# Kernel optimization log

Hardware: AMD Instinct MI355X
Metric: run time of the kernel (lower is better)

## Reference

```python
import jax, jax.numpy as jnp
import numpy as np

B = 1024
D = 128  # in_out_dim


def _lin(k, i, o):
    return jax.random.normal(k, (i, o), jnp.float32) / np.sqrt(i)


def setup_inputs() -> dict:
    key = jax.random.key(0)
    ks = jax.random.split(key, 24)
    inp = {
        'pseudo_t': jax.random.uniform(ks[0], (), jnp.float32),
        'x': jax.random.normal(ks[1], (B, D), jnp.float32),
        'g_x': jax.random.normal(ks[2], (B, 1), jnp.float32),
        'p': jax.random.uniform(ks[3], (B, 1), jnp.float32),
        # GRN encoder: 128->1024->960->896 (Tanh), decoder 896->128
        'gw0': _lin(ks[4], 128, 1024), 'gb0': jnp.zeros((1024,), jnp.float32),
        'gw1': _lin(ks[5], 1024, 960), 'gb1': jnp.zeros((960,), jnp.float32),
        'gw2': _lin(ks[6], 960, 896), 'gb2': jnp.zeros((896,), jnp.float32),
        'gdw': _lin(ks[7], 896, 128), 'gdb': jnp.zeros((128,), jnp.float32),
        # BRD encoder: 129->512->448 (Tanh), decoder 448->1
        'bw0': _lin(ks[8], 129, 512), 'bb0': jnp.zeros((512,), jnp.float32),
        'bw1': _lin(ks[9], 512, 448), 'bb1': jnp.zeros((448,), jnp.float32),
        'bdw': _lin(ks[10], 448, 1), 'bdb': jnp.zeros((1,), jnp.float32),
    }
    return inp


def reference(pseudo_t, x, g_x, p, gw0, gb0, gw1, gb1, gw2, gb2, gdw, gdb,
              bw0, bb0, bw1, bb1, bdw, bdb):
    bsz = x.shape[0]
    x_gene = x[:, :-1]                       # [B, D-1]
    s = jnp.full((bsz, 1), pseudo_t, x.dtype)

    def grn(state):                          # [..., D] -> [..., D]
        h = jnp.tanh(state @ gw0 + gb0)
        h = jnp.tanh(h @ gw1 + gb1)
        h = jnp.tanh(h @ gw2 + gb2)
        return h @ gdw + gdb

    dx_dt = grn(jnp.concatenate([s, x_gene], axis=1))   # [B, D]

    # BRD growth function g(x, t)
    st = jnp.concatenate([s, x], axis=1)                # [B, D+1]
    e = jnp.tanh(st @ bw0 + bb0)
    e = jnp.tanh(e @ bw1 + bb1)
    g = e @ bdw + bdb                                   # [B, 1]

    # trace of d(dx_dt[:, :D-1]) / d(x_gene), per sample (CNF divergence)
    s_scalar = jnp.reshape(pseudo_t, (1,)).astype(x.dtype)

    def f_single(xg_i):                                 # [D-1] -> [D]
        return grn(jnp.concatenate([s_scalar, xg_i]))

    jac = jax.vmap(jax.jacfwd(f_single))(x_gene)        # [B, D, D-1]
    tr = jnp.trace(jac[:, :D - 1, :], axis1=1, axis2=2) # [B]

    dp_dt = g - p * tr[:, None]                         # [B, 1]
    return (dx_dt, g, dp_dt)
```

## Files before the change

kernel.cpp:

```cpp
#include <hip/hip_runtime.h>


typedef __bf16 bf16;
typedef __bf16 bf16x8 __attribute__((ext_vector_type(8)));
typedef float floatx4 __attribute__((ext_vector_type(4)));

#if defined(__has_builtin)
#if __has_builtin(__builtin_amdgcn_global_load_lds)
#define HAVE_GLL 1
#endif
#endif

typedef __attribute__((address_space(3))) char lds_char_t;
typedef __attribute__((address_space(1))) const char gbl_char_t;

__device__ inline void async_load16(const void* gp, void* lp) {
#ifdef HAVE_GLL
  __builtin_amdgcn_global_load_lds((gbl_char_t*)gp, (lds_char_t*)lp, 16, 0, 0);
#else
  *(bf16x8*)lp = *(const bf16x8*)gp;
#endif
}

__device__ inline void stage_async(const bf16* src, long row0, int ld, int kc,
                                   bf16* dst, int wid, int sr8, int cph) {
#pragma unroll
  for (int t = 0; t < 4; ++t) {
    const int r = (wid * 4 + t) * 8 + sr8;
    const int csrc = (cph - r) & 7;
    async_load16(src + (row0 + r) * (size_t)ld + kc + csrc * 8,
                 dst + r * 64 + cph * 8);
  }
}

__device__ inline void mfma_block(const bf16* As, const bf16* Bs,
                                  floatx4 (&acc)[4][4], int wm, int wn,
                                  int l16, int quad) {
#pragma unroll
  for (int ks = 0; ks < 2; ++ks) {
    bf16x8 af[4], bfv[4];
#pragma unroll
    for (int mt = 0; mt < 4; ++mt) {
      const int r = wm * 64 + mt * 16 + l16;
      const int c = (ks * 4 + quad + r) & 7;
      af[mt] = *(const bf16x8*)(As + r * 64 + c * 8);
    }
#pragma unroll
    for (int nt = 0; nt < 4; ++nt) {
      const int r = wn * 64 + nt * 16 + l16;
      const int c = (ks * 4 + quad + r) & 7;
      bfv[nt] = *(const bf16x8*)(Bs + r * 64 + c * 8);
    }
#pragma unroll
    for (int mt = 0; mt < 4; ++mt)
#pragma unroll
      for (int nt = 0; nt < 4; ++nt)
        acc[mt][nt] = __builtin_amdgcn_mfma_f32_16x16x32_bf16(af[mt], bfv[nt], acc[mt][nt], 0, 0, 0);
  }
}

struct TB1 {
  const bf16* A;
  const bf16* w0b;
  const bf16* d0b;
  const bf16* sc;
  bf16* Upr;
  int i0, NT, ch, nTiles;
};

struct TB2 {
  const bf16* A;
  const bf16* Bm;
  const bf16* sc;
  const float* gdw;
  float* tr;
  int i0, NT, ch, nTiles;
};

__device__ __forceinline__ void gemm256(const bf16* Aop, const bf16* Bop,
                                        int m0, int n0, int NT, char* lds,
                                        floatx4 (&acc)[8][4]) {
  const int tid = threadIdx.x;
  const int wid = tid >> 6, lane = tid & 63;
  const int wm = wid & 1, wn = wid >> 1;
  const int quad = lane >> 4, l16 = lane & 15;

  const int sr = tid >> 2;
  const int sg = tid & 3;
  const int csrc = (sg - (sr >> 1)) & 3;
  const bf16* aSrc = Aop + (size_t)(m0 + sr) * 1024 + csrc * 8;
  const bf16* bSrc = Bop + (size_t)(n0 + sr) * 1024 + csrc * 8;

  const int rA = wm * 128 + l16;
  const int rB = wn * 64 + l16;
  const int aOff = rA * 64 + ((quad + (rA >> 1)) & 3) * 16;
  const int bOff = rB * 64 + ((quad + (rB >> 1)) & 3) * 16;

#define STAGE4(hh)                                                             \
  {                                                                            \
    char* db = lds + ((hh) & 3) * 32768;                                       \
    const int kce = (hh) * 32;                                                 \
    async_load16(aSrc + kce, db + tid * 16);                                   \
    async_load16(aSrc + 131072 + kce, db + 8192 + tid * 16);                   \
    async_load16(bSrc + kce, db + 16384 + tid * 16);                           \
    async_load16(bSrc + 131072 + kce, db + 24576 + tid * 16);                  \
  }

#define HALF_COMPUTE(HB)                                                       \
  {                                                                            \
    const char* hb_ = (const char*)(HB);                                       \
    bf16x8 af[8], bv[4];                                                       \
    _Pragma("unroll")                                                          \
    for (int nf = 0; nf < 4; ++nf)                                             \
      bv[nf] = *(const bf16x8*)(hb_ + 16384 + bOff + nf * 1024);               \
    _Pragma("unroll")                                                          \
    for (int mf = 0; mf < 8; ++mf)                                             \
      af[mf] = *(const bf16x8*)(hb_ + aOff + mf * 1024);                       \
    _Pragma("unroll")                                                          \
    for (int mf = 0; mf < 8; ++mf)                                             \
      _Pragma("unroll")                                                        \
      for (int nf = 0; nf < 4; ++nf)                                           \
        acc[mf][nf] = __builtin_amdgcn_mfma_f32_16x16x32_bf16(                 \
            af[mf], bv[nf], acc[mf][nf], 0, 0, 0);                             \
  }

#define VMW(N) asm volatile("s_waitcnt vmcnt(" #N ")" ::: "memory")
#define BARRIER()                                                              \
  asm volatile("s_barrier" ::: "memory");                                      \
  __builtin_amdgcn_sched_barrier(0)

  STAGE4(0);
  STAGE4(1);
  VMW(4);
  BARRIER();

#pragma unroll 2
  for (int t = 0; t < NT; ++t) {
    const int h0 = 2 * t;
    const bool more = (t + 1 < NT);

    if (more) STAGE4(h0 + 2);
    HALF_COMPUTE(lds + (h0 & 3) * 32768);
    if (more) VMW(4); else VMW(0);
    BARRIER();

    if (more) STAGE4(h0 + 3);
    HALF_COMPUTE(lds + ((h0 + 1) & 3) * 32768);
    if (more) {
      VMW(4);
      BARRIER();
    }
  }
#undef STAGE4
#undef HALF_COMPUTE
#undef VMW
#undef BARRIER
}

__device__ __forceinline__ void gemm256_b1(const bf16* Aop, const bf16* w0p,
                                           const bf16* d0p1, const bf16* d0p2,
                                           int m0, int NT, char* lds,
                                           floatx4 (&acc)[8][4]) {
  const int tid = threadIdx.x;
  const int wid = tid >> 6, lane = tid & 63;
  const int wm = wid & 1, wn = wid >> 1;
  const int quad = lane >> 4, l16 = lane & 15;

  const int sr = tid >> 2;
  const int sg = tid & 3;
  const int csrc = (sg - (sr >> 1)) & 3;
  const bf16* aSrc = Aop + (size_t)(m0 + sr) * 1024 + csrc * 8;

  const int rA = wm * 128 + l16;
  const int rB = wn * 64 + l16;
  const int aOff = rA * 64 + ((quad + (rA >> 1)) & 3) * 16;
  const int bOff = rB * 64 + ((quad + (rB >> 1)) & 3) * 16;

#define STAGE1(hh)                                                             \
  {                                                                            \
    char* db = lds + ((hh) & 3) * 32768;                                       \
    const int kce = (hh) * 32;                                                 \
    bf16x8 wv = *(const bf16x8*)(w0p + kce);                                   \
    bf16x8 v1 = *(const bf16x8*)(d0p1 + kce);                                  \
    bf16x8 v2 = *(const bf16x8*)(d0p2 + kce);                                  \
    async_load16(aSrc + kce, db + tid * 16);                                   \
    async_load16(aSrc + 131072 + kce, db + 8192 + tid * 16);                   \
    bf16x8 o1, o2;                                                             \
    _Pragma("unroll")                                                          \
    for (int k = 0; k < 8; ++k) {                                              \
      o1[k] = (bf16)((float)wv[k] * (float)v1[k]);                             \
      o2[k] = (bf16)((float)wv[k] * (float)v2[k]);                             \
    }                                                                          \
    *(bf16x8*)(db + 16384 + tid * 16) = o1;                                    \
    *(bf16x8*)(db + 24576 + tid * 16) = o2;                                    \
  }

#define HALF_COMPUTE(HB)                                                       \
  {                                                                            \
    const char* hb_ = (const char*)(HB);                                       \
    bf16x8 af[8], bv[4];                                                       \
    _Pragma("unroll")                                                          \
    for (int nf = 0; nf < 4; ++nf)                                             \
      bv[nf] = *(const bf16x8*)(hb_ + 16384 + bOff + nf * 1024);               \
    _Pragma("unroll")                                                          \
    for (int mf = 0; mf < 8; ++mf)                                             \
      af[mf] = *(const bf16x8*)(hb_ + aOff + mf * 1024);                       \
    _Pragma("unroll")                                                          \
    for (int mf = 0; mf < 8; ++mf)                                             \
      _Pragma("unroll")                                                        \
      for (int nf = 0; nf < 4; ++nf)                                           \
        acc[mf][nf] = __builtin_amdgcn_mfma_f32_16x16x32_bf16(                 \
            af[mf], bv[nf], acc[mf][nf], 0, 0, 0);                             \
  }

#define VMW(N) asm volatile("s_waitcnt vmcnt(" #N ")" ::: "memory")
#define BARRIER1()                                                             \
  asm volatile("s_waitcnt lgkmcnt(0)\ns_barrier" ::: "memory");                \
  __builtin_amdgcn_sched_barrier(0)

  STAGE1(0);
  STAGE1(1);
  VMW(2);
  BARRIER1();

#pragma unroll 2
  for (int t = 0; t < NT; ++t) {
    const int h0 = 2 * t;
    const bool more = (t + 1 < NT);

    if (more) STAGE1(h0 + 2);
    HALF_COMPUTE(lds + (h0 & 3) * 32768);
    if (more) VMW(2); else VMW(0);
    BARRIER1();

    if (more) STAGE1(h0 + 3);
    HALF_COMPUTE(lds + ((h0 + 1) & 3) * 32768);
    if (more) {
      VMW(2);
      BARRIER1();
    }
  }
#undef STAGE1
#undef HALF_COMPUTE
#undef VMW
#undef BARRIER1
}

__global__ __launch_bounds__(512, 2) void kt8_b1(TB1 p) {
  extern __shared__ __align__(16) char lds[];
  const int bid = blockIdx.x;
  const int nt  = ((bid >> 4) << 3) | (bid & 7);
  const int mtp = (bid >> 3) & 1;
  if (nt >= p.nTiles) return;

  const int tid = threadIdx.x;
  const int wid = tid >> 6, lane = tid & 63;
  const int wm = wid & 1, wn = wid >> 1;
  const int quad = lane >> 4, l16 = lane & 15;
  const long nLim = (long)p.ch * 128;

  const int sr = tid >> 2;
  const int sg = tid & 3;
  const int csrc = (sg - (sr >> 1)) & 3;
  const int wsel = (sr == 127) ? 127 : sr + 1;
  const bf16* w0p  = p.w0b + wsel * 1024 + csrc * 8;
  const bf16* d0p1 = p.d0b + (size_t)(p.i0 + nt * 2) * 1024 + csrc * 8;
  const bf16* d0p2 = d0p1 + 1024;

#pragma unroll 1
  for (int q = 0; q < 2; ++q) {
    const int mt = mtp * 2 + q;
    floatx4 acc[8][4];
#pragma unroll
    for (int a = 0; a < 8; ++a)
#pragma unroll
      for (int b = 0; b < 4; ++b)
#pragma unroll
        for (int r = 0; r < 4; ++r) acc[a][b][r] = 0.0f;

    gemm256_b1(p.A, w0p, d0p1, d0p2, mt * 256, p.NT, lds, acc);

    const int mb = mt * 256 + wm * 128;
#pragma unroll
    for (int nf = 0; nf < 4; ++nf) {
      const long n = (long)nt * 256 + wn * 64 + nf * 16 + l16;
      if (n < nLim) {
        const int ig = p.i0 + (int)(n >> 7);
        const bf16* dp = p.sc + (size_t)ig * 960;
        bf16* urow = p.Upr + (size_t)n * 1024;
#pragma unroll
        for (int mf = 0; mf < 8; ++mf) {
          const int mg = mb + mf * 16 + quad * 4;
          if (mg < 960) {
            union { bf16 h[4]; uint2 u; } o;
#pragma unroll
            for (int r = 0; r < 4; ++r)
              o.h[r] = (bf16)(acc[mf][nf][r] * (float)dp[mg + r]);
            *(uint2*)(urow + mg) = o.u;
          }
        }
      }
    }
  }
}

__global__ __launch_bounds__(512, 2) void kt8_b2(TB2 p) {
  extern __shared__ __align__(16) char lds[];
  const int bid = blockIdx.x;
  const int mt  = (bid >> 3) & 3;
  const int ntp = ((bid >> 5) << 3) | (bid & 7);
  const int npairs = (p.nTiles + 1) >> 1;
  if (ntp >= npairs) return;

  const int tid = threadIdx.x;
  const int wid = tid >> 6, lane = tid & 63;
  const int wm = wid & 1, wn = wid >> 1;
  const int quad = lane >> 4, l16 = lane & 15;
  const long nLim = (long)p.ch * 128;
  const int mb = mt * 256 + wm * 128;

  float sAB[2] = {0.0f, 0.0f};
#pragma unroll 1
  for (int q = 0; q < 2; ++q) {
    const int nt = ntp * 2 + q;
    if (nt >= p.nTiles) break;
    floatx4 acc[8][4];
#pragma unroll
    for (int a = 0; a < 8; ++a)
#pragma unroll
      for (int b = 0; b < 4; ++b)
#pragma unroll
        for (int r = 0; r < 4; ++r) acc[a][b][r] = 0.0f;

    gemm256(p.A, p.Bm, mt * 256, nt * 256, p.NT, lds, acc);

    float s = 0.0f;
#pragma unroll
    for (int nf = 0; nf < 4; ++nf) {
      const long n = (long)nt * 256 + wn * 64 + nf * 16 + l16;
      const int d = (int)(n & 127);
      if (n < nLim && d < 127) {
        const int ig = p.i0 + (int)(n >> 7);
        const bf16* dp = p.sc + (size_t)ig * 896;
#pragma unroll
        for (int mf = 0; mf < 8; ++mf) {
          const int mg = mb + mf * 16 + quad * 4;
          if (mg < 896) {
#pragma unroll
            for (int r = 0; r < 4; ++r) {
              const float w = (float)dp[mg + r] * p.gdw[(mg + r) * 128 + d];
              s += acc[mf][nf][r] * w;
            }
          }
        }
      }
    }
#pragma unroll
    for (int off = 1; off < 64; off <<= 1) s += __shfl_xor(s, off, 64);
    sAB[q] = s;
  }

  float* red = (float*)lds;
  if (lane == 0) { red[wid] = sAB[0]; red[8 + wid] = sAB[1]; }
  __syncthreads();
  const int ig0 = p.i0 + ntp * 4;
  if (tid == 0) {
    atomicAdd(p.tr + ig0, red[0] + red[1] + red[2] + red[3]);
    if (ntp * 2 + 1 < p.nTiles)
      atomicAdd(p.tr + ig0 + 2, red[8] + red[9] + red[10] + red[11]);
  }
  if (tid == 256) {
    atomicAdd(p.tr + ig0 + 1, red[4] + red[5] + red[6] + red[7]);
    if (ntp * 2 + 1 < p.nTiles)
      atomicAdd(p.tr + ig0 + 3, red[12] + red[13] + red[14] + red[15]);
  }
}

struct FArgs {
  const bf16* A; int lda;
  const bf16* Bt; int ldb;
  const float* bias;
  bf16* C; int ldc;
  bf16* D; int ldd;
  float* outF; int ldo;
  int K; int realN; int gridX;
};

template <int ACT>
__device__ inline void fwd_body(const FArgs& p, int bx, bf16* As, bf16* Bs) {
  const int tid  = threadIdx.x;
  const int wid  = tid >> 6, lane = tid & 63;
  const int wm   = wid & 1, wn = wid >> 1;
  const int quad = lane >> 4, l16 = lane & 15;
  const int sr8  = lane >> 3, cph = lane & 7;
  const int m0   = (bx % p.gridX) * 128;
  const int bn0  = (bx / p.gridX) * 128;

  floatx4 acc[4][4];
#pragma unroll
  for (int a = 0; a < 4; ++a)
#pragma unroll
    for (int b = 0; b < 4; ++b)
#pragma unroll
      for (int r = 0; r < 4; ++r) acc[a][b][r] = 0.0f;

  for (int kc = 0; kc < p.K; kc += 64) {
    stage_async(p.A, m0, p.lda, kc, As, wid, sr8, cph);
    stage_async(p.Bt, bn0, p.ldb, kc, Bs, wid, sr8, cph);
    __syncthreads();
    mfma_block(As, Bs, acc, wm, wn, l16, quad);
    __syncthreads();
  }

#pragma unroll
  for (int nt = 0; nt < 4; ++nt) {
    const int ng = bn0 + wn * 64 + nt * 16 + l16;
    const float bv = (ng < p.realN) ? p.bias[ng] : 0.0f;
#pragma unroll
    for (int mt = 0; mt < 4; ++mt)
#pragma unroll
      for (int r = 0; r < 4; ++r) {
        const int i = m0 + wm * 64 + mt * 16 + quad * 4 + r;
        const float v = acc[mt][nt][r] + bv;
        if (ACT) {
          const float t = tanhf(v);
          p.C[(size_t)i * p.ldc + ng] = (ng < p.realN) ? (bf16)t : (bf16)0.0f;
          if (p.D && ng < p.realN)
            p.D[(size_t)i * p.ldd + ng] = (bf16)(1.0f - t * t);
        } else if (ng < p.realN) {
          p.outF[(size_t)i * p.ldo + ng] = v;
        }
      }
  }
}

__global__ __launch_bounds__(256) void kt_fwd2(FArgs a, int na, FArgs b) {
  __shared__ __align__(16) bf16 As[8192];
  __shared__ __align__(16) bf16 Bs[8192];
  const int bx = blockIdx.x;
  if (bx < na) fwd_body<1>(a, bx, As, Bs);
  else         fwd_body<1>(b, bx - na, As, Bs);
}

__global__ __launch_bounds__(256) void kt_fwd1(FArgs a) {
  __shared__ __align__(16) bf16 As[8192];
  __shared__ __align__(16) bf16 Bs[8192];
  fwd_body<1>(a, blockIdx.x, As, Bs);
}

__global__ __launch_bounds__(256) void kt_dxgdot(FArgs a, int na,
                                                 const bf16* e1b, const float* bdw,
                                                 const float* bdb, float* gf,
                                                 float* gout) {
  __shared__ __align__(16) bf16 As[8192];
  __shared__ __align__(16) bf16 Bs[8192];
  const int bx = blockIdx.x;
  if (bx < na) { fwd_body<0>(a, bx, As, Bs); return; }
  const int i = (bx - na) * 4 + (threadIdx.x >> 6);
  const int lane = threadIdx.x & 63;
  float s = 0.0f;
  for (int k = lane; k < 448; k += 64) s += (float)e1b[(size_t)i * 512 + k] * bdw[k];
#pragma unroll
  for (int off = 32; off > 0; off >>= 1) s += __shfl_down(s, off, 64);
  if (lane == 0) {
    const float v = s + bdb[0];
    gf[i] = v;
    gout[i] = v;
  }
}

struct PArgs {
  const float *gw0, *gw1, *gw2, *gdw, *bw0, *bw1, *pt, *x;
  bf16 *gw0b, *gw0t, *gw1t, *gw2t, *gdwt, *bw0t, *bw1t, *Xg, *Xb;
};

__device__ inline void tpose_tile(bf16* dst, const float* src, int R, int C,
                                  int ldd, int tile, int tilesX, float* tl,
                                  int tid) {
  const int r0 = (tile % tilesX) * 64;
  const int c0 = (tile / tilesX) * 64;
  const int tx = tid & 63, ty0 = tid >> 6;
#pragma unroll
  for (int i = 0; i < 16; ++i) {
    const int ty = ty0 + i * 4;
    const int r = r0 + ty, c = c0 + tx;
    tl[ty * 65 + tx] = (r < R && c < C) ? src[(size_t)r * C + c] : 0.0f;
  }
  __syncthreads();
#pragma unroll
  for (int i = 0; i < 16; ++i) {
    const int ty = ty0 + i * 4;
    dst[(size_t)(c0 + ty) * ldd + r0 + tx] = (bf16)tl[tx * 65 + ty];
  }
}

__global__ __launch_bounds__(256) void kt_prep(PArgs p) {
  __shared__ float tl[64 * 65];
  int b = blockIdx.x;
  const int t = threadIdx.x;
  if (b < 512) { p.gw0b[b * 256 + t] = (bf16)p.gw0[b * 256 + t]; return; }
  b -= 512;
  if (b < 768) {
    const int idx = b * 256 + t;
    const int i = idx / 192, c = idx % 192;
    const float s = p.pt[0];
    float vb;
    if (c == 0) vb = s;
    else if (c <= 128) vb = p.x[i * 128 + c - 1];
    else vb = 0.0f;
    p.Xb[i * 192 + c] = (bf16)vb;
    if (c < 128) p.Xg[i * 128 + c] = (bf16)((c == 0) ? s : p.x[i * 128 + c - 1]);
    return;
  }
  b -= 768;
  if (b < 32)  { tpose_tile(p.gw0t, p.gw0, 128, 1024, 128, b, 2, tl, t);  return; }
  b -= 32;
  if (b < 256) { tpose_tile(p.gw1t, p.gw1, 1024, 960, 1024, b, 16, tl, t); return; }
  b -= 256;
  if (b < 256) { tpose_tile(p.gw2t, p.gw2, 960, 896, 1024, b, 16, tl, t); return; }
  b -= 256;
  if (b < 32)  { tpose_tile(p.gdwt, p.gdw, 896, 128, 1024, b, 16, tl, t); return; }
  b -= 32;
  if (b < 24)  { tpose_tile(p.bw0t, p.bw0, 129, 512, 192, b, 3, tl, t);  return; }
  b -= 24;
  if (b < 64)  { tpose_tile(p.bw1t, p.bw1, 512, 448, 512, b, 8, tl, t);  return; }
}

__global__ __launch_bounds__(256) void kt_fin(const float* gf, const float* tr,
                                              const float* pp, float* dp) {
  const int i = blockIdx.x * 256 + threadIdx.x;
  if (i < 1024) dp[i] = gf[i] - pp[i] * tr[i];
}

extern "C" void kernel_launch(void* const* d_in, const int* in_sizes, int n_in,
                              void* d_out, int out_size, void* d_ws, size_t ws_size,
                              hipStream_t stream) {
  const float* pt  = (const float*)d_in[0];
  const float* x   = (const float*)d_in[1];
  const float* pp  = (const float*)d_in[3];
  const float* gw0 = (const float*)d_in[4];
  const float* gb0 = (const float*)d_in[5];
  const float* gw1 = (const float*)d_in[6];
  const float* gb1 = (const float*)d_in[7];
  const float* gw2 = (const float*)d_in[8];
  const float* gb2 = (const float*)d_in[9];
  const float* gdw = (const float*)d_in[10];
  const float* gdb = (const float*)d_in[11];
  const float* bw0 = (const float*)d_in[12];
  const float* bb0 = (const float*)d_in[13];
  const float* bw1 = (const float*)d_in[14];
  const float* bb1 = (const float*)d_in[15];
  const float* bdw = (const float*)d_in[16];
  const float* bdb = (const float*)d_in[17];
  float* out = (float*)d_out;

  static bool s_attr = false;
  if (!s_attr) {
    hipFuncSetAttribute((const void*)kt8_b1,
                        hipFuncAttributeMaxDynamicSharedMemorySize, 131072);
    hipFuncSetAttribute((const void*)kt8_b2,
                        hipFuncAttributeMaxDynamicSharedMemorySize, 131072);
    s_attr = true;
  }

  char* w = (char*)d_ws;
  size_t used = 0;
  auto alloc = [&](size_t nbytes) -> void* {
    void* r = w + used;
    used += (nbytes + 255) & ~(size_t)255;
    return r;
  };
  bf16* gw0b = (bf16*)alloc((size_t)128 * 1024 * 2);
  bf16* gw0t = (bf16*)alloc((size_t)1024 * 128 * 2);
  bf16* gw1t = (bf16*)alloc((size_t)1024 * 1024 * 2);
  bf16* gw2t = (bf16*)alloc((size_t)1024 * 1024 * 2);
  bf16* gdwt = (bf16*)alloc((size_t)128 * 1024 * 2);
  bf16* bw0t = (bf16*)alloc((size_t)512 * 192 * 2);
  bf16* bw1t = (bf16*)alloc((size_t)512 * 512 * 2);
  bf16* Xg   = (bf16*)alloc((size_t)1024 * 128 * 2);
  bf16* Xb   = (bf16*)alloc((size_t)1024 * 192 * 2);
  bf16* h0b  = (bf16*)alloc((size_t)1024 * 1024 * 2);
  bf16* h1b  = (bf16*)alloc((size_t)1024 * 1024 * 2);
  bf16* h2b  = (bf16*)alloc((size_t)1024 * 1024 * 2);
  bf16* e0b  = (bf16*)alloc((size_t)1024 * 512 * 2);
  bf16* e1b  = (bf16*)alloc((size_t)1024 * 512 * 2);
  bf16* d0b  = (bf16*)alloc((size_t)1024 * 1024 * 2);
  bf16* d1b  = (bf16*)alloc((size_t)1024 * 960 * 2);
  bf16* d2b  = (bf16*)alloc((size_t)1024 * 896 * 2);
  float* gf  = (float*)alloc(1024 * 4);
  float* tr  = (float*)alloc(1024 * 4);

  const size_t perSample = (size_t)128 * 1024 * 2;
  size_t avail = (ws_size > used) ? ws_size - used : 0;
  int CH = (int)(avail / perSample);
  if (CH > 256) CH = 256;
  if (CH >= 2) CH &= ~1;
  if (CH < 1) CH = 1;
  bf16* Upr = (bf16*)(w + used);

  hipMemsetAsync(tr, 0, 1024 * 4, stream);

  {
    PArgs a{gw0, gw1, gw2, gdw, bw0, bw1, pt, x,
            gw0b, gw0t, gw1t, gw2t, gdwt, bw0t, bw1t, Xg, Xb};
    kt_prep<<<dim3(1944), 256, 0, stream>>>(a);
  }

  {
    FArgs a{}; a.A = Xg; a.lda = 128; a.Bt = gw0t; a.ldb = 128; a.bias = gb0;
    a.C = h0b; a.ldc = 1024; a.D = d0b; a.ldd = 1024; a.K = 128; a.realN = 1024;
    a.gridX = 8;
    FArgs b{}; b.A = Xb; b.lda = 192; b.Bt = bw0t; b.ldb = 192; b.bias = bb0;
    b.C = e0b; b.ldc = 512; b.K = 192; b.realN = 512; b.gridX = 8;
    kt_fwd2<<<dim3(96), 256, 0, stream>>>(a, 64, b);
  }
  {
    FArgs a{}; a.A = h0b; a.lda = 1024; a.Bt = gw1t; a.ldb = 1024; a.bias = gb1;
    a.C = h1b; a.ldc = 1024; a.D = d1b; a.ldd = 960; a.K = 1024; a.realN = 960;
    a.gridX = 8;
    FArgs b{}; b.A = e0b; b.lda = 512; b.Bt = bw1t; b.ldb = 512; b.bias = bb1;
    b.C = e1b; b.ldc = 512; b.K = 512; b.realN = 448; b.gridX = 8;
    kt_fwd2<<<dim3(96), 256, 0, stream>>>(a, 64, b);
  }
  {
    FArgs a{}; a.A = h1b; a.lda = 1024; a.Bt = gw2t; a.ldb = 1024; a.bias = gb2;
    a.C = h2b; a.ldc = 1024; a.D = d2b; a.ldd = 896; a.K = 1024; a.realN = 896;
    a.gridX = 8;
    kt_fwd1<<<dim3(56), 256, 0, stream>>>(a);
  }
  {
    FArgs a{}; a.A = h2b; a.lda = 1024; a.Bt = gdwt; a.ldb = 1024; a.bias = gdb;
    a.outF = out; a.ldo = 128; a.K = 896; a.realN = 128; a.gridX = 8;
    kt_dxgdot<<<dim3(8 + 256), 256, 0, stream>>>(a, 8, e1b, bdw, bdb, gf, out + 131072);
  }

  for (int i0 = 0; i0 < 1024; i0 += CH) {
    const int ch  = (1024 - i0 < CH) ? (1024 - i0) : CH;
    const int nTiles = (ch * 128 + 255) >> 8;
    const int nT8 = (nTiles + 7) & ~7;
    {
      TB1 a{}; a.A = gw1t; a.w0b = gw0b; a.d0b = d0b; a.sc = d1b; a.Upr = Upr;
      a.i0 = i0; a.NT = 16; a.ch = ch; a.nTiles = nTiles;
      kt8_b1<<<dim3(nT8 * 2), 512, 131072, stream>>>(a);
    }
    {
      const int npairs = (nTiles + 1) >> 1;
      const int np8 = (npairs + 7) & ~7;
      TB2 a{}; a.A = gw2t; a.Bm = Upr; a.sc = d2b; a.gdw = gdw; a.tr = tr;
      a.i0 = i0; a.NT = 15; a.ch = ch; a.nTiles = nTiles;
      kt8_b2<<<dim3(np8 * 4), 512, 131072, stream>>>(a);
    }
  }

  kt_fin<<<dim3(4), 256, 0, stream>>>(gf, tr, pp, out + 132096);
}
```

Baseline: 826.5 us.

## Use double-buffered LDS and one tile per block in Jacobian GEMMs

Replaces the four-slot LDS ring, which kept two half-steps of prefetch in flight, with a two-slot ring that prefetches one half-step ahead and waits on vmcnt(0) every step. LDS per block drops from 128 KB to 64 KB. Each block now computes a single 256x256 output tile instead of looping over two, so the grids are twice as large. This aims to raise occupancy and spread work over more blocks, at the cost of less latency hiding from the shallower prefetch and a full memory wait plus barrier on every half-step.

```diff
diff --git a/kernel.cpp b/kernel.cpp
--- a/kernel.cpp
+++ b/kernel.cpp
@@ -77,6 +77,14 @@
   int i0, NT, ch, nTiles;
 };
 
+#define VMW0() asm volatile("s_waitcnt vmcnt(0)" ::: "memory")
+#define BAR_PLAIN()                                                            \
+  asm volatile("s_barrier" ::: "memory");                                      \
+  __builtin_amdgcn_sched_barrier(0)
+#define BAR_LGKM()                                                             \
+  asm volatile("s_waitcnt lgkmcnt(0)\ns_barrier" ::: "memory");                \
+  __builtin_amdgcn_sched_barrier(0)
+
 __device__ __forceinline__ void gemm256(const bf16* Aop, const bf16* Bop,
                                         int m0, int n0, int NT, char* lds,
                                         floatx4 (&acc)[8][4]) {
@@ -98,7 +106,7 @@
 
 #define STAGE4(hh)                                                             \
   {                                                                            \
-    char* db = lds + ((hh) & 3) * 32768;                                       \
+    char* db = lds + ((hh) & 1) * 32768;                                       \
     const int kce = (hh) * 32;                                                 \
     async_load16(aSrc + kce, db + tid * 16);                                   \
     async_load16(aSrc + 131072 + kce, db + 8192 + tid * 16);                   \
@@ -124,37 +132,20 @@
             af[mf], bv[nf], acc[mf][nf], 0, 0, 0);                             \
   }
 
-#define VMW(N) asm volatile("s_waitcnt vmcnt(" #N ")" ::: "memory")
-#define BARRIER()                                                              \
-  asm volatile("s_barrier" ::: "memory");                                      \
-  __builtin_amdgcn_sched_barrier(0)
-
+  const int H = 2 * NT;
   STAGE4(0);
-  STAGE4(1);
-  VMW(4);
-  BARRIER();
+  VMW0();
+  BAR_PLAIN();
 
 #pragma unroll 2
-  for (int t = 0; t < NT; ++t) {
-    const int h0 = 2 * t;
-    const bool more = (t + 1 < NT);
-
-    if (more) STAGE4(h0 + 2);
-    HALF_COMPUTE(lds + (h0 & 3) * 32768);
-    if (more) VMW(4); else VMW(0);
-    BARRIER();
-
-    if (more) STAGE4(h0 + 3);
-    HALF_COMPUTE(lds + ((h0 + 1) & 3) * 32768);
-    if (more) {
-      VMW(4);
-      BARRIER();
-    }
+  for (int h = 0; h < H; ++h) {
+    if (h + 1 < H) STAGE4(h + 1);
+    HALF_COMPUTE(lds + (h & 1) * 32768);
+    VMW0();
+    BAR_PLAIN();
   }
 #undef STAGE4
 #undef HALF_COMPUTE
-#undef VMW
-#undef BARRIER
 }
 
 __device__ __forceinline__ void gemm256_b1(const bf16* Aop, const bf16* w0p,
@@ -170,6 +161,7 @@
   const int sg = tid & 3;
   const int csrc = (sg - (sr >> 1)) & 3;
   const bf16* aSrc = Aop + (size_t)(m0 + sr) * 1024 + csrc * 8;
+  (void)sg;
 
   const int rA = wm * 128 + l16;
   const int rB = wn * 64 + l16;
@@ -178,7 +170,7 @@
 
 #define STAGE1(hh)                                                             \
   {                                                                            \
-    char* db = lds + ((hh) & 3) * 32768;                                       \
+    char* db = lds + ((hh) & 1) * 32768;                                       \
     const int kce = (hh) * 32;                                                 \
     bf16x8 wv = *(const bf16x8*)(w0p + kce);                                   \
     bf16x8 v1 = *(const bf16x8*)(d0p1 + kce);                                  \
@@ -213,44 +205,27 @@
             af[mf], bv[nf], acc[mf][nf], 0, 0, 0);                             \
   }
 
-#define VMW(N) asm volatile("s_waitcnt vmcnt(" #N ")" ::: "memory")
-#define BARRIER1()                                                             \
-  asm volatile("s_waitcnt lgkmcnt(0)\ns_barrier" ::: "memory");                \
-  __builtin_amdgcn_sched_barrier(0)
-
+  const int H = 2 * NT;
   STAGE1(0);
-  STAGE1(1);
-  VMW(2);
-  BARRIER1();
+  VMW0();
+  BAR_LGKM();
 
 #pragma unroll 2
-  for (int t = 0; t < NT; ++t) {
-    const int h0 = 2 * t;
-    const bool more = (t + 1 < NT);
-
-    if (more) STAGE1(h0 + 2);
-    HALF_COMPUTE(lds + (h0 & 3) * 32768);
-    if (more) VMW(2); else VMW(0);
-    BARRIER1();
-
-    if (more) STAGE1(h0 + 3);
-    HALF_COMPUTE(lds + ((h0 + 1) & 3) * 32768);
-    if (more) {
-      VMW(2);
-      BARRIER1();
-    }
+  for (int h = 0; h < H; ++h) {
+    if (h + 1 < H) STAGE1(h + 1);
+    HALF_COMPUTE(lds + (h & 1) * 32768);
+    VMW0();
+    BAR_LGKM();
   }
 #undef STAGE1
 #undef HALF_COMPUTE
-#undef VMW
-#undef BARRIER1
 }
 
 __global__ __launch_bounds__(512, 2) void kt8_b1(TB1 p) {
   extern __shared__ __align__(16) char lds[];
   const int bid = blockIdx.x;
-  const int nt  = ((bid >> 4) << 3) | (bid & 7);
-  const int mtp = (bid >> 3) & 1;
+  const int mt  = (bid >> 3) & 3;
+  const int nt  = ((bid >> 5) << 3) | (bid & 7);
   if (nt >= p.nTiles) return;
 
   const int tid = threadIdx.x;
@@ -267,37 +242,33 @@
   const bf16* d0p1 = p.d0b + (size_t)(p.i0 + nt * 2) * 1024 + csrc * 8;
   const bf16* d0p2 = d0p1 + 1024;
 
-#pragma unroll 1
-  for (int q = 0; q < 2; ++q) {
-    const int mt = mtp * 2 + q;
-    floatx4 acc[8][4];
-#pragma unroll
-    for (int a = 0; a < 8; ++a)
-#pragma unroll
-      for (int b = 0; b < 4; ++b)
-#pragma unroll
-        for (int r = 0; r < 4; ++r) acc[a][b][r] = 0.0f;
-
-    gemm256_b1(p.A, w0p, d0p1, d0p2, mt * 256, p.NT, lds, acc);
-
-    const int mb = mt * 256 + wm * 128;
-#pragma unroll
-    for (int nf = 0; nf < 4; ++nf) {
-      const long n = (long)nt * 256 + wn * 64 + nf * 16 + l16;
-      if (n < nLim) {
-        const int ig = p.i0 + (int)(n >> 7);
-        const bf16* dp = p.sc + (size_t)ig * 960;
-        bf16* urow = p.Upr + (size_t)n * 1024;
-#pragma unroll
-        for (int mf = 0; mf < 8; ++mf) {
-          const int mg = mb + mf * 16 + quad * 4;
-          if (mg < 960) {
-            union { bf16 h[4]; uint2 u; } o;
-#pragma unroll
-            for (int r = 0; r < 4; ++r)
-              o.h[r] = (bf16)(acc[mf][nf][r] * (float)dp[mg + r]);
-            *(uint2*)(urow + mg) = o.u;
-          }
+  floatx4 acc[8][4];
+#pragma unroll
+  for (int a = 0; a < 8; ++a)
+#pragma unroll
+    for (int b = 0; b < 4; ++b)
+#pragma unroll
+      for (int r = 0; r < 4; ++r) acc[a][b][r] = 0.0f;
+
+  gemm256_b1(p.A, w0p, d0p1, d0p2, mt * 256, p.NT, lds, acc);
+
+  const int mb = mt * 256 + wm * 128;
+#pragma unroll
+  for (int nf = 0; nf < 4; ++nf) {
+    const long n = (long)nt * 256 + wn * 64 + nf * 16 + l16;
+    if (n < nLim) {
+      const int ig = p.i0 + (int)(n >> 7);
+      const bf16* dp = p.sc + (size_t)ig * 960;
+      bf16* urow = p.Upr + (size_t)n * 1024;
+#pragma unroll
+      for (int mf = 0; mf < 8; ++mf) {
+        const int mg = mb + mf * 16 + quad * 4;
+        if (mg < 960) {
+          union { bf16 h[4]; uint2 u; } o;
+#pragma unroll
+          for (int r = 0; r < 4; ++r)
+            o.h[r] = (bf16)(acc[mf][nf][r] * (float)dp[mg + r]);
+          *(uint2*)(urow + mg) = o.u;
         }
       }
     }
@@ -308,72 +279,57 @@
   extern __shared__ __align__(16) char lds[];
   const int bid = blockIdx.x;
   const int mt  = (bid >> 3) & 3;
-  const int ntp = ((bid >> 5) << 3) | (bid & 7);
-  const int npairs = (p.nTiles + 1) >> 1;
-  if (ntp >= npairs) return;
-
+  const int nt  = ((bid >> 5) << 3) | (bid & 7);
   const int tid = threadIdx.x;
+  if (nt >= p.nTiles) return;
+
   const int wid = tid >> 6, lane = tid & 63;
   const int wm = wid & 1, wn = wid >> 1;
   const int quad = lane >> 4, l16 = lane & 15;
   const long nLim = (long)p.ch * 128;
   const int mb = mt * 256 + wm * 128;
 
-  float sAB[2] = {0.0f, 0.0f};
-#pragma unroll 1
-  for (int q = 0; q < 2; ++q) {
-    const int nt = ntp * 2 + q;
-    if (nt >= p.nTiles) break;
-    floatx4 acc[8][4];
-#pragma unroll
-    for (int a = 0; a < 8; ++a)
-#pragma unroll
-      for (int b = 0; b < 4; ++b)
-#pragma unroll
-        for (int r = 0; r < 4; ++r) acc[a][b][r] = 0.0f;
-
-    gemm256(p.A, p.Bm, mt * 256, nt * 256, p.NT, lds, acc);
-
-    float s = 0.0f;
-#pragma unroll
-    for (int nf = 0; nf < 4; ++nf) {
-      const long n = (long)nt * 256 + wn * 64 + nf * 16 + l16;
-      const int d = (int)(n & 127);
-      if (n < nLim && d < 127) {
-        const int ig = p.i0 + (int)(n >> 7);
-        const bf16* dp = p.sc + (size_t)ig * 896;
-#pragma unroll
-        for (int mf = 0; mf < 8; ++mf) {
-          const int mg = mb + mf * 16 + quad * 4;
-          if (mg < 896) {
-#pragma unroll
-            for (int r = 0; r < 4; ++r) {
-              const float w = (float)dp[mg + r] * p.gdw[(mg + r) * 128 + d];
-              s += acc[mf][nf][r] * w;
-            }
+  floatx4 acc[8][4];
+#pragma unroll
+  for (int a = 0; a < 8; ++a)
+#pragma unroll
+    for (int b = 0; b < 4; ++b)
+#pragma unroll
+      for (int r = 0; r < 4; ++r) acc[a][b][r] = 0.0f;
+
+  gemm256(p.A, p.Bm, mt * 256, nt * 256, p.NT, lds, acc);
+
+  float s = 0.0f;
+#pragma unroll
+  for (int nf = 0; nf < 4; ++nf) {
+    const long n = (long)nt * 256 + wn * 64 + nf * 16 + l16;
+    const int d = (int)(n & 127);
+    if (n < nLim && d < 127) {
+      const int ig = p.i0 + (int)(n >> 7);
+      const bf16* dp = p.sc + (size_t)ig * 896;
+#pragma unroll
+      for (int mf = 0; mf < 8; ++mf) {
+        const int mg = mb + mf * 16 + quad * 4;
+        if (mg < 896) {
+#pragma unroll
+          for (int r = 0; r < 4; ++r) {
+            const float w = (float)dp[mg + r] * p.gdw[(mg + r) * 128 + d];
+            s += acc[mf][nf][r] * w;
           }
         }
       }
     }
-#pragma unroll
-    for (int off = 1; off < 64; off <<= 1) s += __shfl_xor(s, off, 64);
-    sAB[q] = s;
-  }
-
+  }
+#pragma unroll
+  for (int off = 1; off < 64; off <<= 1) s += __shfl_xor(s, off, 64);
   float* red = (float*)lds;
-  if (lane == 0) { red[wid] = sAB[0]; red[8 + wid] = sAB[1]; }
+  if (lane == 0) red[wid] = s;
   __syncthreads();
-  const int ig0 = p.i0 + ntp * 4;
-  if (tid == 0) {
-    atomicAdd(p.tr + ig0, red[0] + red[1] + red[2] + red[3]);
-    if (ntp * 2 + 1 < p.nTiles)
-      atomicAdd(p.tr + ig0 + 2, red[8] + red[9] + red[10] + red[11]);
-  }
-  if (tid == 256) {
-    atomicAdd(p.tr + ig0 + 1, red[4] + red[5] + red[6] + red[7]);
-    if (ntp * 2 + 1 < p.nTiles)
-      atomicAdd(p.tr + ig0 + 3, red[12] + red[13] + red[14] + red[15]);
-  }
+  const int igA = p.i0 + nt * 2;
+  if (tid == 0)
+    atomicAdd(p.tr + igA, red[0] + red[1] + red[2] + red[3]);
+  if (tid == 256 && nt * 2 + 1 < p.ch)
+    atomicAdd(p.tr + igA + 1, red[4] + red[5] + red[6] + red[7]);
 }
 
 struct FArgs {
@@ -557,9 +513,9 @@
   static bool s_attr = false;
   if (!s_attr) {
     hipFuncSetAttribute((const void*)kt8_b1,
-                        hipFuncAttributeMaxDynamicSharedMemorySize, 131072);
+                        hipFuncAttributeMaxDynamicSharedMemorySize, 65536);
     hipFuncSetAttribute((const void*)kt8_b2,
-                        hipFuncAttributeMaxDynamicSharedMemorySize, 131072);
+                        hipFuncAttributeMaxDynamicSharedMemorySize, 65536);
     s_attr = true;
   }
 
@@ -641,14 +597,12 @@
     {
       TB1 a{}; a.A = gw1t; a.w0b = gw0b; a.d0b = d0b; a.sc = d1b; a.Upr = Upr;
       a.i0 = i0; a.NT = 16; a.ch = ch; a.nTiles = nTiles;
-      kt8_b1<<<dim3(nT8 * 2), 512, 131072, stream>>>(a);
+      kt8_b1<<<dim3(nT8 * 4), 512, 65536, stream>>>(a);
     }
     {
-      const int npairs = (nTiles + 1) >> 1;
-      const int np8 = (npairs + 7) & ~7;
       TB2 a{}; a.A = gw2t; a.Bm = Upr; a.sc = d2b; a.gdw = gdw; a.tr = tr;
       a.i0 = i0; a.NT = 15; a.ch = ch; a.nTiles = nTiles;
-      kt8_b2<<<dim3(np8 * 4), 512, 131072, stream>>>(a);
+      kt8_b2<<<dim3(nT8 * 4), 512, 65536, stream>>>(a);
     }
   }
 
```

Result: slower. 866.9 us (+4.9%).
